# Optimization experiments

Measured on AMD Instinct MI355X. Metric: run time of the kernel, lower is better.

The kernel has to match this reference:

```python
import jax, jax.numpy as jnp
import numpy as np

H = 16      # query heads
KVH = 4     # kv heads
G = H // KVH


def _split_heads(x, nh, d):
    # [b, P, C, nh*d] -> [b, nh, P, C, d]
    b, P, C, _ = x.shape
    return jnp.transpose(x.reshape(b, P, C, nh, d), (0, 3, 1, 2, 4))


def _rel_shift(x, P, T):
    # x: [b, h, T, P]  (Transformer-XL style relative shift via memory reinterpretation)
    b, h = x.shape[:2]
    xv = x.reshape(b, h, P, T)
    xp = jnp.concatenate([jnp.zeros((b, h, P, 1), x.dtype), xv], axis=-1)  # [b,h,P,T+1]
    return xp.reshape(b, h, T + 1, P)[:, :, 1:, :]


def _rel_shift_chan(x, C, T):
    # x: [b, h, T, C]; gather with index (C-1 - |i-j|) tiled over T rows
    i = jnp.arange(C)
    idx = (C - 1) - jnp.abs(i[:, None] - i[None, :])          # [C, C]
    tiled = jnp.tile(idx, (T // C, 1))[None, None]            # [1,1,T,C]
    return jnp.take_along_axis(x, jnp.broadcast_to(tiled, x.shape), axis=-1)


def _forward(hidden_states, positional_embedding, channel_embedding,
             Wq, Wkv, Wpos, Wchan, Wproj, attn_bias):
    b, P, C, E = hidden_states.shape
    D = E // H
    EKV = D * KVH
    T = P * C

    q = hidden_states @ Wq                                    # [b,P,C,E]
    kv = hidden_states @ Wkv                                  # [b,P,C,2*EKV]
    gk_raw, v_raw = kv[..., :EKV], kv[..., EKV:]
    tk_raw = positional_embedding @ Wpos                      # [1,P,1,EKV]
    ck_raw = channel_embedding @ Wchan                        # [1,1,C,EKV]

    q = _split_heads(q, H, D)                                 # [b,H,P,C,D]
    gk = jnp.repeat(_split_heads(gk_raw, KVH, D), G, axis=1)  # [b,H,P,C,D]
    v = jnp.repeat(_split_heads(v_raw, KVH, D), G, axis=1)    # [b,H,P,C,D]
    tk = jnp.repeat(_split_heads(tk_raw, KVH, D), G, axis=1)[:, :, :, 0, :]  # [1,H,P,D]
    ck = jnp.repeat(_split_heads(ck_raw, KVH, D), G, axis=1)[:, :, 0, :, :]  # [1,H,C,D]

    gb, tb, cb = (jnp.repeat(attn_bias[i * EKV:(i + 1) * EKV].reshape(KVH, D), G, axis=0)
                  [None, :, None, None, :] for i in range(3))  # each [1,H,1,1,D]

    qg = (q + gb).reshape(b, H, T, D)
    qt = (q + tb).reshape(b, H, T, D)
    qc = (q + cb).reshape(b, H, T, D)

    gk_f = gk.reshape(b, H, T, D)
    global_att = jnp.einsum('bhtd,bhsd->bhts', qg, gk_f)      # [b,H,T,T]
    time_att = jnp.einsum('bhtd,bhpd->bhtp', qt, tk)          # [b,H,T,P]
    chan_att = jnp.einsum('bhtd,bhcd->bhtc', qc, ck)          # [b,H,T,C]

    time_att = _rel_shift(time_att, P, T)
    chan_att = _rel_shift_chan(chan_att, C, T)

    # repeat_channel + repeat_time -> both [b,H,T,T]
    attn = jnp.repeat(time_att, C, axis=-1) + jnp.tile(chan_att, (1, 1, 1, P))

    # global window mask (+/-10 in time, all-true for last chan_len rows)
    pm = jnp.tril(jnp.ones((P, P), bool), 10) & jnp.triu(jnp.ones((P, P), bool), -10)
    wm = jnp.repeat(jnp.repeat(pm, C, axis=0), C, axis=1)
    wm = wm.at[-C:].set(True)
    attn = attn + jnp.where(wm, global_att, jnp.zeros((), attn.dtype))

    attn = attn / jnp.asarray(D ** 0.5, attn.dtype)           # scale_attn_weights

    causal = jnp.repeat(jnp.repeat(jnp.tril(jnp.ones((P, P), bool)), C, axis=0), C, axis=1)
    attn = jnp.where(causal, attn, jnp.finfo(attn.dtype).min)

    w = jax.nn.softmax(attn, axis=-1)                         # [b,H,T,T]
    out = jnp.einsum('bhts,bhsd->bhtd', w, v.reshape(b, H, T, D)).reshape(b, H, P, C, D)

    # merge heads: [b,H,P,C,D] -> [b,P,C,E], then output proj
    out = jnp.transpose(out, (0, 2, 3, 1, 4)).reshape(b, P, C, E)
    return out @ Wproj


def setup_inputs() -> dict:
    key = jax.random.key(0)
    ks = jax.random.split(key, 9)
    B, P, C, E, EKV = 2, 128, 8, 1024, 256
    s = 0.02
    return {
        'hidden_states': jax.random.normal(ks[0], (B, P, C, E), jnp.float32),
        'positional_embedding': jax.random.normal(ks[1], (1, P, 1, E), jnp.float32),
        'channel_embedding': jax.random.normal(ks[2], (1, 1, C, E), jnp.float32),
        'Wq': jax.random.normal(ks[3], (E, E), jnp.float32) * s,
        'Wkv': jax.random.normal(ks[4], (E, 2 * EKV), jnp.float32) * s,
        'Wpos': jax.random.normal(ks[5], (E, EKV), jnp.float32) * s,
        'Wchan': jax.random.normal(ks[6], (E, EKV), jnp.float32) * s,
        'Wproj': jax.random.normal(ks[7], (E, E), jnp.float32) * s,
        'attn_bias': jax.random.normal(ks[8], (3 * EKV,), jnp.float32) * s,
    }


def reference(hidden_states, positional_embedding, channel_embedding,
              Wq, Wkv, Wpos, Wchan, Wproj, attn_bias):
    return _forward(hidden_states, positional_embedding, channel_embedding,
                    Wq, Wkv, Wpos, Wchan, Wproj, attn_bias)
```

## Files before the change

### kernel.cpp

```cpp
#include <hip/hip_runtime.h>
#include <hip/hip_bf16.h>

#define BB 2
#define PP 128
#define CC 8
#define EE 1024
#define HH 16
#define KVHH 4
#define DD 64
#define TT 1024
#define EKVV 256

typedef unsigned short u16;
typedef unsigned int u32;
typedef __attribute__((ext_vector_type(8))) short bf16x8;
typedef __attribute__((ext_vector_type(4))) float f32x4;

__device__ __forceinline__ float b2f(u16 u) {
    u32 x = ((u32)u) << 16;
    return __uint_as_float(x);
}
__device__ __forceinline__ u16 f2b(float f) {
    u32 x = __float_as_uint(f);
    u32 r = (x + 0x7FFFu + ((x >> 16) & 1u)) >> 16;
    return (u16)r;
}

template <int CTRL>
__device__ __forceinline__ float dpp_mv(float v) {
    return __int_as_float(__builtin_amdgcn_update_dpp(
        __float_as_int(v), __float_as_int(v), CTRL, 0xF, 0xF, true));
}
__device__ __forceinline__ float red_max16(float v) {
    v = fmaxf(v, dpp_mv<0xB1>(v));
    v = fmaxf(v, dpp_mv<0x4E>(v));
    v = fmaxf(v, dpp_mv<0x141>(v));
    v = fmaxf(v, dpp_mv<0x140>(v));
    return v;
}
__device__ __forceinline__ float red_sum16(float v) {
    v += dpp_mv<0xB1>(v);
    v += dpp_mv<0x4E>(v);
    v += dpp_mv<0x141>(v);
    v += dpp_mv<0x140>(v);
    return v;
}

#define GLL16(gp, lp)                                                          \
    __builtin_amdgcn_global_load_lds(                                          \
        (__attribute__((address_space(1))) void*)(gp),                         \
        (__attribute__((address_space(3))) void*)(lp), 16, 0, 0)

__global__ __launch_bounds__(256) void k_prep(const float* __restrict__ hidden,
                                              const float* __restrict__ Wq,
                                              const float* __restrict__ Wkv,
                                              const float* __restrict__ Wproj,
                                              const float* __restrict__ pos,
                                              const float* __restrict__ chan,
                                              const float* __restrict__ Wpos,
                                              const float* __restrict__ Wchan,
                                              u16* __restrict__ hb,
                                              u16* __restrict__ btq,
                                              u16* __restrict__ btp,
                                              float* __restrict__ tkb,
                                              float* __restrict__ ckb) {
    __shared__ __align__(16) char sm[8704];
    int bid = blockIdx.x;
    int tid = threadIdx.x;

    if (bid < 192) {
        int tile = bid >> 4, kh = bid & 15;
        float (*As)[68] = (float (*)[68])sm;
        float (*Bs)[68] = (float (*)[68])(sm + 4352);
        const float* A; const float* B; float* C; int M, m0, n0;
        if (tile < 8) { A = pos;  B = Wpos;  C = tkb + kh * 32768; M = 128; m0 = (tile >> 2) * 64; n0 = (tile & 3) * 64; }
        else          { A = chan; B = Wchan; C = ckb + kh * 2048;  M = 8;   m0 = 0;               n0 = (tile - 8) * 64; }
        int tx = tid & 15, ty = tid >> 4;
        float acc[4][4];
#pragma unroll
        for (int r = 0; r < 4; r++)
#pragma unroll
            for (int c = 0; c < 4; c++) acc[r][c] = 0.f;
        int am = tid >> 2, ak = (tid & 3) << 2;
        int bk = tid >> 4, bn = (tid & 15) << 2;
        for (int k0 = kh * 64; k0 < kh * 64 + 64; k0 += 16) {
            int row = m0 + am;
            float4 av;
            if (row < M) av = *reinterpret_cast<const float4*>(A + (size_t)row * 1024 + k0 + ak);
            else av = make_float4(0.f, 0.f, 0.f, 0.f);
            As[ak + 0][am] = av.x;
            As[ak + 1][am] = av.y;
            As[ak + 2][am] = av.z;
            As[ak + 3][am] = av.w;
            float4 bv = *reinterpret_cast<const float4*>(B + (size_t)(k0 + bk) * 256 + n0 + bn);
            Bs[bk][bn + 0] = bv.x;
            Bs[bk][bn + 1] = bv.y;
            Bs[bk][bn + 2] = bv.z;
            Bs[bk][bn + 3] = bv.w;
            __syncthreads();
#pragma unroll
            for (int kk = 0; kk < 16; kk++) {
                float4 a4 = *reinterpret_cast<const float4*>(&As[kk][ty << 2]);
                float4 b4 = *reinterpret_cast<const float4*>(&Bs[kk][tx << 2]);
                acc[0][0] += a4.x * b4.x; acc[0][1] += a4.x * b4.y; acc[0][2] += a4.x * b4.z; acc[0][3] += a4.x * b4.w;
                acc[1][0] += a4.y * b4.x; acc[1][1] += a4.y * b4.y; acc[1][2] += a4.y * b4.z; acc[1][3] += a4.y * b4.w;
                acc[2][0] += a4.z * b4.x; acc[2][1] += a4.z * b4.y; acc[2][2] += a4.z * b4.z; acc[2][3] += a4.z * b4.w;
                acc[3][0] += a4.w * b4.x; acc[3][1] += a4.w * b4.y; acc[3][2] += a4.w * b4.z; acc[3][3] += a4.w * b4.w;
            }
            __syncthreads();
        }
#pragma unroll
        for (int r = 0; r < 4; r++) {
            int row = m0 + (ty << 2) + r;
            if (row < M) {
#pragma unroll
                for (int c = 0; c < 4; c++) {
                    int col = n0 + (tx << 2) + c;
                    C[(size_t)row * 256 + col] = acc[r][c];
                }
            }
        }
        return;
    }
    bid -= 192;
    if (bid < 1024) {
        int base = (bid * 256 + tid) * 8;
        float4 a0 = *(const float4*)(hidden + base);
        float4 a1 = *(const float4*)(hidden + base + 4);
        u16 o[8] = {f2b(a0.x), f2b(a0.y), f2b(a0.z), f2b(a0.w),
                    f2b(a1.x), f2b(a1.y), f2b(a1.z), f2b(a1.w)};
        *(uint4*)(hb + base) = *(uint4*)o;
        return;
    }
    bid -= 1024;
    const float* W;
    u16* out;
    int N, tk, tn;
    if (bid < 1024) {
        W = Wq; out = btq; N = 1024; tk = bid >> 5; tn = bid & 31;
    } else if (bid < 1536) {
        int b2 = bid - 1024;
        W = Wkv; out = btq + 1024 * 1024; N = 512; tk = b2 >> 4; tn = b2 & 15;
    } else {
        int b2 = bid - 1536;
        W = Wproj; out = btp; N = 1024; tk = b2 >> 5; tn = b2 & 31;
    }
    float (*ts)[33] = (float (*)[33])sm;
    int r = tid >> 3, c4 = (tid & 7) << 2;
    float4 v = *(const float4*)(W + (size_t)(tk * 32 + r) * N + tn * 32 + c4);
    ts[r][c4 + 0] = v.x;
    ts[r][c4 + 1] = v.y;
    ts[r][c4 + 2] = v.z;
    ts[r][c4 + 3] = v.w;
    __syncthreads();
    u16 o[4] = {f2b(ts[c4 + 0][r]), f2b(ts[c4 + 1][r]),
                f2b(ts[c4 + 2][r]), f2b(ts[c4 + 3][r])};
    *(ushort4*)(out + (size_t)(tn * 32 + r) * 1024 + tk * 32 + c4) = *(ushort4*)o;
}

__global__ __launch_bounds__(256) void mgemm_qkv3(const u16* __restrict__ Ab,
                                                  const u16* __restrict__ BT,
                                                  u16* __restrict__ qout,
                                                  u16* __restrict__ kvout,
                                                  u16* __restrict__ vtb,
                                                  const float* __restrict__ tkb,
                                                  const float* __restrict__ ckb,
                                                  u16* __restrict__ tkr,
                                                  float* __restrict__ ckr) {
    __shared__ __align__(16) u16 As[2][64 * 64];
    __shared__ __align__(16) u16 Bs[2][64 * 64];
    int tid = threadIdx.x;
    int ntile = blockIdx.x;

    if (ntile == 24) {
        int y = blockIdx.y;
        if (y >= 16) return;
        int p = y * 8 + (tid >> 5), col = (tid & 31) << 3;
        float s0 = 0.f, s1 = 0.f, s2 = 0.f, s3 = 0.f,
              s4 = 0.f, s5 = 0.f, s6 = 0.f, s7 = 0.f;
#pragma unroll
        for (int sl = 0; sl < 16; sl++) {
            const float* tp = tkb + sl * 32768 + p * 256 + col;
            float4 a0 = *(const float4*)(tp);
            float4 a1 = *(const float4*)(tp + 4);
            s0 += a0.x; s1 += a0.y; s2 += a0.z; s3 += a0.w;
            s4 += a1.x; s5 += a1.y; s6 += a1.z; s7 += a1.w;
        }
        u16 o[8] = {f2b(s0), f2b(s1), f2b(s2), f2b(s3),
                    f2b(s4), f2b(s5), f2b(s6), f2b(s7)};
        int kvh = col >> 6, d = col & 63;
        *(uint4*)(tkr + kvh * 8192 + p * 64 + d) = *(uint4*)o;
        if (y == 0) {
            int c = tid >> 5, cc = (tid & 31) << 3;
            float t[8];
#pragma unroll
            for (int j = 0; j < 8; j++) t[j] = 0.f;
#pragma unroll
            for (int sl = 0; sl < 16; sl++) {
                const float* cp = ckb + sl * 2048 + c * 256 + cc;
                float4 a0 = *(const float4*)(cp);
                float4 a1 = *(const float4*)(cp + 4);
                t[0] += a0.x; t[1] += a0.y; t[2] += a0.z; t[3] += a0.w;
                t[4] += a1.x; t[5] += a1.y; t[6] += a1.z; t[7] += a1.w;
            }
            int kvh2 = cc >> 6, d2 = cc & 63;
            float* op = ckr + kvh2 * 512 + c * 64 + d2;
            *(float4*)(op)     = make_float4(t[0], t[1], t[2], t[3]);
            *(float4*)(op + 4) = make_float4(t[4], t[5], t[6], t[7]);
        }
        return;
    }

    int m0 = blockIdx.y * 64;
    int n0g = (ntile < 16) ? ntile * 64 : 1024 + (ntile - 16) * 64;

    int lane = tid & 63, wave = tid >> 6;
    int r16 = lane & 15, quad = lane >> 4;
    int mb = (wave >> 1) * 32, nb = (wave & 1) * 32;
    int srow = tid >> 3;
    int skg = (((tid & 7) ^ (srow & 7)) << 3);

#define STAGE_QKV(buf, k0)                                                         \
    do {                                                                           \
        GLL16(Ab + (size_t)(m0 + srow) * 1024 + (k0) + skg,       As[buf] + tid * 8);        \
        GLL16(Ab + (size_t)(m0 + srow + 32) * 1024 + (k0) + skg,  As[buf] + (tid + 256) * 8);\
        GLL16(BT + (size_t)(n0g + srow) * 1024 + (k0) + skg,      Bs[buf] + tid * 8);        \
        GLL16(BT + (size_t)(n0g + srow + 32) * 1024 + (k0) + skg, Bs[buf] + (tid + 256) * 8);\
    } while (0)

    f32x4 acc[2][2];
#pragma unroll
    for (int mt = 0; mt < 2; mt++)
#pragma unroll
        for (int nt = 0; nt < 2; nt++) acc[mt][nt] = (f32x4){0.f, 0.f, 0.f, 0.f};

    STAGE_QKV(0, 0);
    __syncthreads();
    int cur = 0;
    for (int k0 = 0; k0 < 1024; k0 += 64) {
        if (k0 + 64 < 1024) STAGE_QKV(cur ^ 1, k0 + 64);
#pragma unroll
        for (int ks = 0; ks < 2; ks++) {
            bf16x8 af[2], bfr[2];
#pragma unroll
            for (int mt = 0; mt < 2; mt++) {
                int r = mb + mt * 16 + r16;
                af[mt] = *(const bf16x8*)(As[cur] + r * 64 +
                                          ((ks * 32 + quad * 8) ^ ((r & 7) << 3)));
            }
#pragma unroll
            for (int nt = 0; nt < 2; nt++) {
                int r = nb + nt * 16 + r16;
                bfr[nt] = *(const bf16x8*)(Bs[cur] + r * 64 +
                                           ((ks * 32 + quad * 8) ^ ((r & 7) << 3)));
            }
#pragma unroll
            for (int mt = 0; mt < 2; mt++)
#pragma unroll
                for (int nt = 0; nt < 2; nt++)
                    acc[mt][nt] = __builtin_amdgcn_mfma_f32_16x16x32_bf16(af[mt], bfr[nt], acc[mt][nt], 0, 0, 0);
        }
        __syncthreads();
        cur ^= 1;
    }
    if (ntile < 20) {
        u16* Cout; int BN, n0;
        if (ntile < 16) { Cout = qout;  BN = 1024; n0 = ntile * 64; }
        else            { Cout = kvout; BN = 512;  n0 = (ntile - 16) * 64; }
#pragma unroll
        for (int mt = 0; mt < 2; mt++)
#pragma unroll
            for (int nt = 0; nt < 2; nt++)
#pragma unroll
                for (int rg = 0; rg < 4; rg++) {
                    int row = m0 + mb + mt * 16 + quad * 4 + rg;
                    int col = n0 + nb + nt * 16 + r16;
                    Cout[(size_t)row * BN + col] = f2b(acc[mt][nt][rg]);
                }
    } else {
        int n0 = (ntile - 16) * 64;
#pragma unroll
        for (int mt = 0; mt < 2; mt++)
#pragma unroll
            for (int nt = 0; nt < 2; nt++)
#pragma unroll
                for (int rg = 0; rg < 4; rg++) {
                    int row = m0 + mb + mt * 16 + quad * 4 + rg;
                    int col = n0 + nb + nt * 16 + r16;
                    int bb = row >> 10, s = row & 1023;
                    vtb[((size_t)bb << 18) + ((size_t)(col - 256) << 10) + s] =
                        f2b(acc[mt][nt][rg]);
                }
    }
#undef STAGE_QKV
}

__global__ __launch_bounds__(256) void mgemm_proj3(const u16* __restrict__ Ab,
                                                   const u16* __restrict__ BT,
                                                   float* __restrict__ Cf) {
    __shared__ __align__(16) u16 As[2][64 * 64];
    __shared__ __align__(16) u16 Bs[2][64 * 64];
    int tid = threadIdx.x;
    int n0 = blockIdx.x * 64;
    int m0 = blockIdx.y * 64;

    int lane = tid & 63, wave = tid >> 6;
    int r16 = lane & 15, quad = lane >> 4;
    int mb = (wave >> 1) * 32, nb = (wave & 1) * 32;
    int srow = tid >> 3;
    int skg = (((tid & 7) ^ (srow & 7)) << 3);

#define STAGE_PRJ(buf, k0)                                                         \
    do {                                                                           \
        GLL16(Ab + (size_t)(m0 + srow) * 1024 + (k0) + skg,      As[buf] + tid * 8);        \
        GLL16(Ab + (size_t)(m0 + srow + 32) * 1024 + (k0) + skg, As[buf] + (tid + 256) * 8);\
        GLL16(BT + (size_t)(n0 + srow) * 1024 + (k0) + skg,      Bs[buf] + tid * 8);        \
        GLL16(BT + (size_t)(n0 + srow + 32) * 1024 + (k0) + skg, Bs[buf] + (tid + 256) * 8);\
    } while (0)

    f32x4 acc[2][2];
#pragma unroll
    for (int mt = 0; mt < 2; mt++)
#pragma unroll
        for (int nt = 0; nt < 2; nt++) acc[mt][nt] = (f32x4){0.f, 0.f, 0.f, 0.f};

    STAGE_PRJ(0, 0);
    __syncthreads();
    int cur = 0;
    for (int k0 = 0; k0 < 1024; k0 += 64) {
        if (k0 + 64 < 1024) STAGE_PRJ(cur ^ 1, k0 + 64);
#pragma unroll
        for (int ks = 0; ks < 2; ks++) {
            bf16x8 af[2], bfr[2];
#pragma unroll
            for (int mt = 0; mt < 2; mt++) {
                int r = mb + mt * 16 + r16;
                af[mt] = *(const bf16x8*)(As[cur] + r * 64 +
                                          ((ks * 32 + quad * 8) ^ ((r & 7) << 3)));
            }
#pragma unroll
            for (int nt = 0; nt < 2; nt++) {
                int r = nb + nt * 16 + r16;
                bfr[nt] = *(const bf16x8*)(Bs[cur] + r * 64 +
                                           ((ks * 32 + quad * 8) ^ ((r & 7) << 3)));
            }
#pragma unroll
            for (int mt = 0; mt < 2; mt++)
#pragma unroll
                for (int nt = 0; nt < 2; nt++)
                    acc[mt][nt] = __builtin_amdgcn_mfma_f32_16x16x32_bf16(af[mt], bfr[nt], acc[mt][nt], 0, 0, 0);
        }
        __syncthreads();
        cur ^= 1;
    }
#pragma unroll
    for (int mt = 0; mt < 2; mt++)
#pragma unroll
        for (int nt = 0; nt < 2; nt++)
#pragma unroll
            for (int rg = 0; rg < 4; rg++) {
                int row = m0 + mb + mt * 16 + quad * 4 + rg;
                int col = n0 + nb + nt * 16 + r16;
                Cf[(size_t)row * 1024 + col] = acc[mt][nt][rg];
            }
#undef STAGE_PRJ
}

__global__ __launch_bounds__(256, 3) void k_att4(const u16* __restrict__ qb,
                                                 const u16* __restrict__ kvb,
                                                 const u16* __restrict__ vt,
                                                 const u16* __restrict__ tkr,
                                                 const float* __restrict__ ckr,
                                                 const float* __restrict__ bias,
                                                 u16* __restrict__ A2,
                                                 float* __restrict__ pacc,
                                                 float* __restrict__ pml) {
    __shared__ __align__(16) char smem[49664];
    u16*   taX  = (u16*)(smem);
    u16*   qg   = (u16*)(smem);
    u16*   tkS  = (u16*)(smem + 17408);
    u16*   Kst  = (u16*)(smem + 17408);
    u16*   Vst  = (u16*)(smem + 26624);
    u16*   Pst  = (u16*)(smem + 35840);
    float* csA  = (float*)(smem + 45056);
    float* cks  = (float*)(smem + 47104);
    float* cbmg = (float*)(smem + 49152);
    float* tbv  = (float*)(smem + 49408);

    static const unsigned char Gt[24] = {15,15,14,14,13,13,12,12,
                                          7, 6,11,11,10,10, 9, 5,
                                          0, 1, 2, 8, 3, 9, 8, 4};
    static const unsigned char Mt[24] = {0,1,1,0,0,1,1,0,
                                         2,2,0,1,1,0,0,2,
                                         2,2,2,0,2,1,1,2};

    int tid = threadIdx.x;
    int lane = tid & 63, wave = tid >> 6;
    int r16 = lane & 15, quad = lane >> 4;
    int h = blockIdx.y, b = blockIdx.z;
    int g = Gt[blockIdx.x], mode = Mt[blockIdx.x];
    int kvh = h >> 2;
    int t0 = g * 64;
    int hn = (g + 1) >> 1;
    int clo = (mode == 1) ? hn : 0;
    int chi = (mode == 0) ? hn : (g + 1);

    const u16* vptr = vt + ((size_t)(b * KVHH + kvh)) * DD * TT
                    + (size_t)(tid >> 3) * TT + ((tid & 7) << 3);
    const u16* kptr = kvb + ((size_t)(b * TT) + (tid >> 3)) * (2 * EKVV)
                    + kvh * 64 + ((tid & 7) << 3);

    uint4 V0g, V1g, K0g, K1g;
    bool pk_next;

#define PRE(c0p)                                                               \
    do {                                                                       \
        V0g = *(const uint4*)(vptr + (c0p));                                   \
        V1g = *(const uint4*)(vptr + 32 * TT + (c0p));                         \
        pk_next = (g == 15) || ((c0p) + 136 > g * 64);                         \
        if (pk_next) {                                                         \
            const u16* kp_ = kptr + (size_t)(c0p) * (2 * EKVV);                \
            K0g = *(const uint4*)(kp_);                                        \
            K1g = *(const uint4*)(kp_ + 32 * 2 * EKVV);                        \
        }                                                                      \
    } while (0)

    PRE(clo * 64);

#pragma unroll
    for (int i = 0; i < 2; i++) {
        int idx = tid + i * 256;
        int row = idx >> 3, dg = (idx & 7) << 3;
        uint4 u = *(const uint4*)(qb + ((size_t)(b * TT + t0 + row)) * EE + h * 64 + dg);
        u16 tmp[8]; *(uint4*)tmp = u;
        u16 o[8];
#pragma unroll
        for (int j = 0; j < 8; j++) o[j] = f2b(b2f(tmp[j]) + bias[kvh * 64 + dg + j]);
        *(uint4*)(qg + row * 72 + dg) = *(uint4*)o;
    }
    if (tid < 64) {
        cbmg[tid] = bias[2 * EKVV + kvh * 64 + tid] - bias[kvh * 64 + tid];
        tbv[tid]  = bias[EKVV + kvh * 64 + tid];
    }
#pragma unroll
    for (int i = 0; i < 2; i++) {
        int idx = tid + i * 256;
        cks[idx] = ckr[kvh * 512 + idx];
    }
    __syncthreads();

    {
        int row = tid >> 2, cA = (tid & 3) << 1;
        int rm8 = row & 7;
        int d0 = rm8 - cA;       if (d0 < 0) d0 = -d0;
        int d1 = rm8 - (cA + 1); if (d1 < 0) d1 = -d1;
        const float* k0p = cks + (7 - d0) * 64;
        const float* k1p = cks + (7 - d1) * 64;
        float a0 = 0.f, a1 = 0.f;
#pragma unroll 8
        for (int d = 0; d < 64; d++) {
            float qv = b2f(qg[row * 72 + d]) + cbmg[d];
            a0 += qv * k0p[d];
            a1 += qv * k1p[d];
        }
        csA[row * 8 + cA] = a0;
        csA[row * 8 + cA + 1] = a1;
    }

    bf16x8 aq0 = *(const bf16x8*)(qg + (wave * 16 + r16) * 72 + quad * 8);
    bf16x8 aq1 = *(const bf16x8*)(qg + (wave * 16 + r16) * 72 + 32 + quad * 8);
    bf16x8 aqt0, aqt1;
    {
        const u16* qrow = qb + ((size_t)(b * TT + t0 + wave * 16 + r16)) * EE + h * 64;
        uint4 u0 = *(const uint4*)(qrow + quad * 8);
        uint4 u1 = *(const uint4*)(qrow + 32 + quad * 8);
        u16 t0v[8], t1v[8]; *(uint4*)t0v = u0; *(uint4*)t1v = u1;
        u16 o0[8], o1[8];
#pragma unroll
        for (int j = 0; j < 8; j++) {
            o0[j] = f2b(b2f(t0v[j]) + tbv[quad * 8 + j]);
            o1[j] = f2b(b2f(t1v[j]) + tbv[32 + quad * 8 + j]);
        }
        aqt0 = *(bf16x8*)o0;
        aqt1 = *(bf16x8*)o1;
    }

    {
        const u16* tkp = tkr + kvh * 8192;
#pragma unroll
        for (int i = 0; i < 4; i++) {
            int idx = tid + i * 256;
            int p = idx >> 3, dg = (idx & 7) << 3;
            *(uint4*)(tkS + p * 72 + dg) = *(const uint4*)(tkp + p * 64 + dg);
        }
    }
    __syncthreads();

    int rpi_w = (t0 >> 3) + wave * 2 + (quad >> 1);
    int xsh = rpi_w - 127;
#pragma unroll
    for (int nt = 0; nt < 8; nt++) {
        const u16* kp = tkS + (nt * 16 + r16) * 72 + quad * 8;
        bf16x8 b0 = *(const bf16x8*)(kp);
        bf16x8 b1 = *(const bf16x8*)(kp + 32);
        f32x4 a = {0.f, 0.f, 0.f, 0.f};
        a = __builtin_amdgcn_mfma_f32_16x16x32_bf16(aqt0, b0, a, 0, 0, 0);
        a = __builtin_amdgcn_mfma_f32_16x16x32_bf16(aqt1, b1, a, 0, 0, 0);
        int x = nt * 16 + r16 + xsh;
        if (x >= 0) {
            u16 o4[4] = {f2b(a[0]), f2b(a[1]), f2b(a[2]), f2b(a[3])};
            *(ushort4*)(taX + x * 68 + wave * 16 + quad * 4) = *(ushort4*)o4;
        }
    }

    float m[4], l[4];
    f32x4 accv[4];
#pragma unroll
    for (int rg = 0; rg < 4; rg++) { m[rg] = -1.0e30f; l[rg] = 0.f; }
#pragma unroll
    for (int nt = 0; nt < 4; nt++) accv[nt] = (f32x4){0.f, 0.f, 0.f, 0.f};

    int rowbase = wave * 16 + quad * 4;
    int rpi[4];
#pragma unroll
    for (int rg = 0; rg < 4; rg++) rpi[rg] = (t0 + rowbase + rg) >> 3;

    for (int ci = clo; ci < chi; ci++) {
        int c0 = ci * 64;
        bool pk = pk_next;
        __syncthreads();
        {
            u16* vw = Vst + (tid >> 3) * 72 + ((tid & 7) << 3);
            *(uint4*)(vw)           = V0g;
            *(uint4*)(vw + 32 * 72) = V1g;
            if (pk) {
                u16* kw = Kst + (tid >> 3) * 72 + ((tid & 7) << 3);
                *(uint4*)(kw)           = K0g;
                *(uint4*)(kw + 32 * 72) = K1g;
            }
        }
        if (ci + 1 < chi) PRE((ci + 1) * 64);
        __syncthreads();

        bool pkq = (c0 + 136 - 16 * wave > g * 64) || (g == 15 && wave == 3);
        f32x4 sc[4];
        if (pkq) {
            __builtin_amdgcn_s_setprio(1);
#pragma unroll
            for (int nt = 0; nt < 4; nt++) {
                const u16* kp = Kst + (nt * 16 + r16) * 72 + quad * 8;
                bf16x8 b0 = *(const bf16x8*)(kp);
                bf16x8 b1 = *(const bf16x8*)(kp + 32);
                f32x4 a = {0.f, 0.f, 0.f, 0.f};
                a = __builtin_amdgcn_mfma_f32_16x16x32_bf16(aq0, b0, a, 0, 0, 0);
                a = __builtin_amdgcn_mfma_f32_16x16x32_bf16(aq1, b1, a, 0, 0, 0);
                sc[nt] = a;
            }
            __builtin_amdgcn_s_setprio(0);
        } else {
#pragma unroll
            for (int nt = 0; nt < 4; nt++) sc[nt] = (f32x4){0.f, 0.f, 0.f, 0.f};
        }

        float csr[4];
#pragma unroll
        for (int rg = 0; rg < 4; rg++) csr[rg] = csA[(rowbase + rg) * 8 + (r16 & 7)];
        int c08 = c0 >> 3;
#pragma unroll
        for (int nt = 0; nt < 4; nt++) {
            int spi = c08 + 2 * nt + (r16 >> 3);
            ushort4 t4 = *(const ushort4*)(taX + spi * 68 + rowbase);
            float tsv[4] = {b2f(t4.x), b2f(t4.y), b2f(t4.z), b2f(t4.w)};
#pragma unroll
            for (int rg = 0; rg < 4; rg++) {
                bool win = (rpi[rg] == 127) || (rpi[rg] - spi <= 10);
                float scv = ((win ? sc[nt][rg] : 0.f) + tsv[rg] + csr[rg]) * 0.125f;
                sc[nt][rg] = (spi <= rpi[rg]) ? scv : -1.0e30f;
            }
        }

        float cm[4], alpha[4], psum[4];
#pragma unroll
        for (int rg = 0; rg < 4; rg++) {
            float v = sc[0][rg];
#pragma unroll
            for (int nt = 1; nt < 4; nt++) v = fmaxf(v, sc[nt][rg]);
            v = red_max16(v);
            float mn = fmaxf(m[rg], v);
            alpha[rg] = __expf(m[rg] - mn);
            m[rg] = mn;
            cm[rg] = mn;
        }
#pragma unroll
        for (int rg = 0; rg < 4; rg++) psum[rg] = 0.f;
#pragma unroll
        for (int nt = 0; nt < 4; nt++)
#pragma unroll
            for (int rg = 0; rg < 4; rg++) {
                float e = __expf(sc[nt][rg] - cm[rg]);
                sc[nt][rg] = e;
                psum[rg] += e;
            }
#pragma unroll
        for (int rg = 0; rg < 4; rg++) {
            psum[rg] = red_sum16(psum[rg]);
            l[rg] = l[rg] * alpha[rg] + psum[rg];
        }
#pragma unroll
        for (int nt = 0; nt < 4; nt++)
#pragma unroll
            for (int rg = 0; rg < 4; rg++) accv[nt][rg] *= alpha[rg];

#pragma unroll
        for (int nt = 0; nt < 4; nt++)
#pragma unroll
            for (int rg = 0; rg < 4; rg++)
                Pst[(rowbase + rg) * 72 + nt * 16 + r16] = f2b(sc[nt][rg]);

        __builtin_amdgcn_s_setprio(1);
#pragma unroll
        for (int ks = 0; ks < 2; ks++) {
            bf16x8 ap = *(const bf16x8*)(Pst + (wave * 16 + r16) * 72 + ks * 32 + quad * 8);
#pragma unroll
            for (int nt = 0; nt < 4; nt++) {
                bf16x8 bv = *(const bf16x8*)(Vst + (nt * 16 + r16) * 72 + ks * 32 + quad * 8);
                accv[nt] = __builtin_amdgcn_mfma_f32_16x16x32_bf16(ap, bv, accv[nt], 0, 0, 0);
            }
        }
        __builtin_amdgcn_s_setprio(0);
    }
#undef PRE

    if (mode == 2) {
#pragma unroll
        for (int nt = 0; nt < 4; nt++)
#pragma unroll
            for (int rg = 0; rg < 4; rg++) {
                int rt = t0 + rowbase + rg;
                A2[((size_t)(b * TT + rt)) * EE + h * 64 + nt * 16 + r16] =
                    f2b(accv[nt][rg] / l[rg]);
            }
    } else {
        int slot = ((b * 16 + h) * 8 + (g - 8)) * 2 + mode;
        float* pa = pacc + (size_t)slot * 4096;
#pragma unroll
        for (int nt = 0; nt < 4; nt++)
#pragma unroll
            for (int rg = 0; rg < 4; rg++)
                pa[(rowbase + rg) * 64 + nt * 16 + r16] = accv[nt][rg];
        if (r16 == 0) {
#pragma unroll
            for (int rg = 0; rg < 4; rg++) {
                pml[slot * 128 + rowbase + rg]      = m[rg];
                pml[slot * 128 + 64 + rowbase + rg] = l[rg];
            }
        }
    }
}

__global__ __launch_bounds__(256) void k_merge(const float* __restrict__ pacc,
                                               const float* __restrict__ pml,
                                               u16* __restrict__ A2) {
    int tid = threadIdx.x;
    int x = blockIdx.x, h = blockIdx.y, b = blockIdx.z;
    int g = 8 + x;
    int slot = ((b * 16 + h) * 8 + x) * 2;
    const float* a0 = pacc + (size_t)slot * 4096;
    const float* a1 = a0 + 4096;
    const float* ml0 = pml + slot * 128;
    const float* ml1 = ml0 + 128;
    int row = tid >> 2, seg = (tid & 3) << 4;
    float m0 = ml0[row], l0 = ml0[64 + row];
    float m1 = ml1[row], l1 = ml1[64 + row];
    float M = fmaxf(m0, m1);
    float e0 = __expf(m0 - M), e1 = __expf(m1 - M);
    float inv = 1.f / (l0 * e0 + l1 * e1);
    u16 o[16];
#pragma unroll
    for (int j0 = 0; j0 < 16; j0 += 4) {
        float4 v0 = *(const float4*)(a0 + row * 64 + seg + j0);
        float4 v1 = *(const float4*)(a1 + row * 64 + seg + j0);
        o[j0 + 0] = f2b((v0.x * e0 + v1.x * e1) * inv);
        o[j0 + 1] = f2b((v0.y * e0 + v1.y * e1) * inv);
        o[j0 + 2] = f2b((v0.z * e0 + v1.z * e1) * inv);
        o[j0 + 3] = f2b((v0.w * e0 + v1.w * e1) * inv);
    }
    int rt = g * 64 + row;
    u16* outp = A2 + ((size_t)(b * TT + rt)) * EE + h * 64 + seg;
    *(uint4*)(outp)     = *(uint4*)o;
    *(uint4*)(outp + 8) = *(uint4*)(o + 8);
}

extern "C" void kernel_launch(void* const* d_in, const int* in_sizes, int n_in,
                              void* d_out, int out_size, void* d_ws, size_t ws_size,
                              hipStream_t stream) {
    const float* hidden = (const float*)d_in[0];
    const float* pos    = (const float*)d_in[1];
    const float* chan   = (const float*)d_in[2];
    const float* Wq     = (const float*)d_in[3];
    const float* Wkv    = (const float*)d_in[4];
    const float* Wpos   = (const float*)d_in[5];
    const float* Wchan  = (const float*)d_in[6];
    const float* Wproj  = (const float*)d_in[7];
    const float* bias   = (const float*)d_in[8];

    u16* qb    = (u16*)d_ws;
    u16* kvb   = qb + 2097152;
    u16* A2    = kvb + 1048576;
    u16* vt    = A2 + 2097152;
    u16* hb    = vt + 524288;
    u16* btq   = hb + 2097152;
    u16* btp   = btq + 1572864;
    u16* tkr   = btp + 1048576;
    float* tkb = (float*)(tkr + 32768);
    float* ckb = tkb + 524288;
    float* ckr = ckb + 32768;
    float* pacc = ckr + 2048;
    float* pml  = pacc + 2097152;

    dim3 blk(256);
    k_prep<<<3776, blk, 0, stream>>>(hidden, Wq, Wkv, Wproj, pos, chan, Wpos, Wchan,
                                     hb, btq, btp, tkb, ckb);
    mgemm_qkv3<<<dim3(25, 32), blk, 0, stream>>>(hb, btq, qb, kvb, vt,
                                                 tkb, ckb, tkr, ckr);
    k_att4<<<dim3(24, 16, 2), blk, 0, stream>>>(qb, kvb, vt, tkr, ckr, bias, A2,
                                                pacc, pml);
    k_merge<<<dim3(8, 16, 2), blk, 0, stream>>>(pacc, pml, A2);
    mgemm_proj3<<<dim3(16, 32), blk, 0, stream>>>(A2, btp, (float*)d_out);
}
```

Baseline: 145.9 us.

## Fuse split-KV merge into projection GEMM, skip idle time-key tiles, lazy rescale

Removes the separate merge kernel by having the output projection GEMM combine the two partial attention accumulators on the fly while staging its A tiles, for row blocks that used split processing. The attention kernel also skips time-key MFMA tiles whose shifted columns fall outside the block's channel range. It adds a lazy online-softmax rescale that only updates the running max when it grows by more than a threshold. The fused staging replaces async global-to-LDS loads with synchronous fp32 loads, exp and convert work inside the GEMM loop, and the merge is recomputed by each of the 16 column blocks.

```diff
diff --git a/kernel.cpp b/kernel.cpp
--- a/kernel.cpp
+++ b/kernel.cpp
@@ -297,12 +297,17 @@
 
 __global__ __launch_bounds__(256) void mgemm_proj3(const u16* __restrict__ Ab,
                                                    const u16* __restrict__ BT,
+                                                   const float* __restrict__ pacc,
+                                                   const float* __restrict__ pml,
                                                    float* __restrict__ Cf) {
     __shared__ __align__(16) u16 As[2][64 * 64];
     __shared__ __align__(16) u16 Bs[2][64 * 64];
     int tid = threadIdx.x;
     int n0 = blockIdx.x * 64;
     int m0 = blockIdx.y * 64;
+    int bb = m0 >> 10, gg = (m0 & 1023) >> 6;
+    bool merged = gg >= 8;
+    int slotbase = bb * 256 + (gg - 8) * 2;
 
     int lane = tid & 63, wave = tid >> 6;
     int r16 = lane & 15, quad = lane >> 4;
@@ -310,25 +315,65 @@
     int srow = tid >> 3;
     int skg = (((tid & 7) ^ (srow & 7)) << 3);
 
-#define STAGE_PRJ(buf, k0)                                                         \
+#define STAGE_B(buf, k0)                                                           \
+    do {                                                                           \
+        GLL16(BT + (size_t)(n0 + srow) * 1024 + (k0) + skg,      Bs[buf] + tid * 8);        \
+        GLL16(BT + (size_t)(n0 + srow + 32) * 1024 + (k0) + skg, Bs[buf] + (tid + 256) * 8);\
+    } while (0)
+
+#define STAGE_A_DIRECT(buf, k0)                                                    \
     do {                                                                           \
         GLL16(Ab + (size_t)(m0 + srow) * 1024 + (k0) + skg,      As[buf] + tid * 8);        \
         GLL16(Ab + (size_t)(m0 + srow + 32) * 1024 + (k0) + skg, As[buf] + (tid + 256) * 8);\
-        GLL16(BT + (size_t)(n0 + srow) * 1024 + (k0) + skg,      Bs[buf] + tid * 8);        \
-        GLL16(BT + (size_t)(n0 + srow + 32) * 1024 + (k0) + skg, Bs[buf] + (tid + 256) * 8);\
     } while (0)
 
+#define STAGE_A_MERGED(buf, k0)                                                    \
+    do {                                                                           \
+        int slot_ = slotbase + ((k0) >> 6) * 16;                                   \
+        const float* a0_ = pacc + (size_t)slot_ * 4096;                            \
+        const float* mlp_ = pml + slot_ * 128;                                     \
+        _Pragma("unroll")                                                          \
+        for (int rr = 0; rr < 2; rr++) {                                           \
+            int r_ = srow + rr * 32;                                               \
+            float m0v = mlp_[r_],       l0v = mlp_[64 + r_];                       \
+            float m1v = mlp_[128 + r_], l1v = mlp_[192 + r_];                      \
+            float M_ = fmaxf(m0v, m1v);                                            \
+            float e0_ = __expf(m0v - M_), e1_ = __expf(m1v - M_);                  \
+            float inv_ = 1.f / (l0v * e0_ + l1v * e1_);                            \
+            const float* p0_ = a0_ + r_ * 64 + skg;                                \
+            const float* p1_ = p0_ + 4096;                                         \
+            float4 x0 = *(const float4*)(p0_);                                     \
+            float4 x1 = *(const float4*)(p0_ + 4);                                 \
+            float4 y0 = *(const float4*)(p1_);                                     \
+            float4 y1 = *(const float4*)(p1_ + 4);                                 \
+            u16 o_[8] = {f2b((x0.x * e0_ + y0.x * e1_) * inv_),                    \
+                         f2b((x0.y * e0_ + y0.y * e1_) * inv_),                    \
+                         f2b((x0.z * e0_ + y0.z * e1_) * inv_),                    \
+                         f2b((x0.w * e0_ + y0.w * e1_) * inv_),                    \
+                         f2b((x1.x * e0_ + y1.x * e1_) * inv_),                    \
+                         f2b((x1.y * e0_ + y1.y * e1_) * inv_),                    \
+                         f2b((x1.z * e0_ + y1.z * e1_) * inv_),                    \
+                         f2b((x1.w * e0_ + y1.w * e1_) * inv_)};                   \
+            *(uint4*)(As[buf] + (tid + rr * 256) * 8) = *(uint4*)o_;               \
+        }                                                                          \
+    } while (0)
+
     f32x4 acc[2][2];
 #pragma unroll
     for (int mt = 0; mt < 2; mt++)
 #pragma unroll
         for (int nt = 0; nt < 2; nt++) acc[mt][nt] = (f32x4){0.f, 0.f, 0.f, 0.f};
 
-    STAGE_PRJ(0, 0);
+    STAGE_B(0, 0);
+    if (merged) STAGE_A_MERGED(0, 0); else STAGE_A_DIRECT(0, 0);
     __syncthreads();
     int cur = 0;
     for (int k0 = 0; k0 < 1024; k0 += 64) {
-        if (k0 + 64 < 1024) STAGE_PRJ(cur ^ 1, k0 + 64);
+        if (k0 + 64 < 1024) {
+            STAGE_B(cur ^ 1, k0 + 64);
+            if (merged) STAGE_A_MERGED(cur ^ 1, k0 + 64);
+            else STAGE_A_DIRECT(cur ^ 1, k0 + 64);
+        }
 #pragma unroll
         for (int ks = 0; ks < 2; ks++) {
             bf16x8 af[2], bfr[2];
@@ -363,7 +408,9 @@
                 int col = n0 + nb + nt * 16 + r16;
                 Cf[(size_t)row * 1024 + col] = acc[mt][nt][rg];
             }
-#undef STAGE_PRJ
+#undef STAGE_B
+#undef STAGE_A_DIRECT
+#undef STAGE_A_MERGED
 }
 
 __global__ __launch_bounds__(256, 3) void k_att4(const u16* __restrict__ qb,
@@ -498,8 +545,12 @@
 
     int rpi_w = (t0 >> 3) + wave * 2 + (quad >> 1);
     int xsh = rpi_w - 127;
+    int xshw = (t0 >> 3) + wave * 2 - 127;
+    int blo = 8 * clo, bhi = 8 * chi;
 #pragma unroll
     for (int nt = 0; nt < 8; nt++) {
+        int bl = nt * 16 + xshw;
+        if (bl + 17 <= blo || bl >= bhi) continue;
         const u16* kp = tkS + (nt * 16 + r16) * 72 + quad * 8;
         bf16x8 b0 = *(const bf16x8*)(kp);
         bf16x8 b1 = *(const bf16x8*)(kp + 32);
@@ -580,16 +631,21 @@
         }
 
         float cm[4], alpha[4], psum[4];
+        bool anyresc = false;
 #pragma unroll
         for (int rg = 0; rg < 4; rg++) {
             float v = sc[0][rg];
 #pragma unroll
             for (int nt = 1; nt < 4; nt++) v = fmaxf(v, sc[nt][rg]);
             v = red_max16(v);
-            float mn = fmaxf(m[rg], v);
-            alpha[rg] = __expf(m[rg] - mn);
-            m[rg] = mn;
-            cm[rg] = mn;
+            if (v > m[rg] + 8.f) {
+                alpha[rg] = __expf(m[rg] - v);
+                m[rg] = v;
+                anyresc = true;
+            } else {
+                alpha[rg] = 1.f;
+            }
+            cm[rg] = m[rg];
         }
 #pragma unroll
         for (int rg = 0; rg < 4; rg++) psum[rg] = 0.f;
@@ -606,10 +662,12 @@
             psum[rg] = red_sum16(psum[rg]);
             l[rg] = l[rg] * alpha[rg] + psum[rg];
         }
-#pragma unroll
-        for (int nt = 0; nt < 4; nt++)
-#pragma unroll
-            for (int rg = 0; rg < 4; rg++) accv[nt][rg] *= alpha[rg];
+        if (anyresc) {
+#pragma unroll
+            for (int nt = 0; nt < 4; nt++)
+#pragma unroll
+                for (int rg = 0; rg < 4; rg++) accv[nt][rg] *= alpha[rg];
+        }
 
 #pragma unroll
         for (int nt = 0; nt < 4; nt++)
@@ -656,39 +714,6 @@
             }
         }
     }
-}
-
-__global__ __launch_bounds__(256) void k_merge(const float* __restrict__ pacc,
-                                               const float* __restrict__ pml,
-                                               u16* __restrict__ A2) {
-    int tid = threadIdx.x;
-    int x = blockIdx.x, h = blockIdx.y, b = blockIdx.z;
-    int g = 8 + x;
-    int slot = ((b * 16 + h) * 8 + x) * 2;
-    const float* a0 = pacc + (size_t)slot * 4096;
-    const float* a1 = a0 + 4096;
-    const float* ml0 = pml + slot * 128;
-    const float* ml1 = ml0 + 128;
-    int row = tid >> 2, seg = (tid & 3) << 4;
-    float m0 = ml0[row], l0 = ml0[64 + row];
-    float m1 = ml1[row], l1 = ml1[64 + row];
-    float M = fmaxf(m0, m1);
-    float e0 = __expf(m0 - M), e1 = __expf(m1 - M);
-    float inv = 1.f / (l0 * e0 + l1 * e1);
-    u16 o[16];
-#pragma unroll
-    for (int j0 = 0; j0 < 16; j0 += 4) {
-        float4 v0 = *(const float4*)(a0 + row * 64 + seg + j0);
-        float4 v1 = *(const float4*)(a1 + row * 64 + seg + j0);
-        o[j0 + 0] = f2b((v0.x * e0 + v1.x * e1) * inv);
-        o[j0 + 1] = f2b((v0.y * e0 + v1.y * e1) * inv);
-        o[j0 + 2] = f2b((v0.z * e0 + v1.z * e1) * inv);
-        o[j0 + 3] = f2b((v0.w * e0 + v1.w * e1) * inv);
-    }
-    int rt = g * 64 + row;
-    u16* outp = A2 + ((size_t)(b * TT + rt)) * EE + h * 64 + seg;
-    *(uint4*)(outp)     = *(uint4*)o;
-    *(uint4*)(outp + 8) = *(uint4*)(o + 8);
 }
 
 extern "C" void kernel_launch(void* const* d_in, const int* in_sizes, int n_in,
@@ -725,6 +750,5 @@
                                                  tkb, ckb, tkr, ckr);
     k_att4<<<dim3(24, 16, 2), blk, 0, stream>>>(qb, kvb, vt, tkr, ckr, bias, A2,
                                                 pacc, pml);
-    k_merge<<<dim3(8, 16, 2), blk, 0, stream>>>(pacc, pml, A2);
-    mgemm_proj3<<<dim3(16, 32), blk, 0, stream>>>(A2, btp, (float*)d_out);
-}
+    mgemm_proj3<<<dim3(16, 32), blk, 0, stream>>>(A2, btp, pacc, pml, (float*)d_out);
+}
```

After: 151.4 us. 3.8% more time.
